# Performance work log

Measured on AMD Instinct MI355X. Metric: run time of the kernel, lower is better.

The kernel has to match this reference:

```python
import jax, jax.numpy as jnp
import numpy as np

B, T = 256, 256
D_TEXT, D_AUDIO, D_VISION = 300, 74, 35
D = D_TEXT + D_AUDIO + D_VISION  # 409
H = 1024
CELL = 512
OUT = 1


def setup_inputs() -> dict:
    key = jax.random.key(0)
    ks = jax.random.split(key, 8)
    s_ih = 1.0 / np.sqrt(H)
    return {
        "x_text": jax.random.normal(ks[0], (B, T, D_TEXT), jnp.float32),
        "x_audio": jax.random.normal(ks[1], (B, T, D_AUDIO), jnp.float32),
        "x_vision": jax.random.normal(ks[2], (B, T, D_VISION), jnp.float32),
        "W_ih": jax.random.normal(ks[3], (4 * H, D), jnp.float32) * s_ih,
        "W_hh": jax.random.normal(ks[4], (4 * H, H), jnp.float32) * s_ih,
        "b_ih": jnp.zeros((4 * H,), jnp.float32),
        "b_hh": jnp.zeros((4 * H,), jnp.float32),
        "W1": jax.random.normal(ks[5], (CELL, H), jnp.float32) / np.sqrt(H),
        "b1": jnp.zeros((CELL,), jnp.float32),
        "W2": jax.random.normal(ks[6], (OUT, CELL), jnp.float32) / np.sqrt(CELL),
        "b2": jnp.zeros((OUT,), jnp.float32),
    }


def _lstm_mlp(x_text, x_audio, x_vision, W_ih, W_hh, b_ih, b_hh, W1, b1, W2, b2):
    # concat modalities along feature dim: [B, T, D]
    x = jnp.concatenate([x_text, x_audio, x_vision], axis=2)
    b = x.shape[0]
    h0 = jnp.zeros((b, H), x.dtype)
    c0 = jnp.zeros((b, H), x.dtype)
    # precompute input-to-gate projection for all timesteps: [T, B, 4H]
    xg = jnp.einsum('btd,gd->tbg', x, W_ih) + (b_ih + b_hh)

    def step(carry, xg_t):
        h, c = carry
        gates = xg_t + h @ W_hh.T  # [B, 4H]
        i, f, g, o = jnp.split(gates, 4, axis=-1)  # PyTorch LSTMCell gate order
        i = jax.nn.sigmoid(i)
        f = jax.nn.sigmoid(f)
        g = jnp.tanh(g)
        o = jax.nn.sigmoid(o)
        c = f * c + i * g
        h = o * jnp.tanh(c)
        return (h, c), None

    (h_last, _), _ = jax.lax.scan(step, (h0, c0), xg)
    # SimpleNet: Linear -> ReLU -> Dropout(eval: identity) -> Linear
    hidden = jax.nn.relu(h_last @ W1.T + b1)
    return hidden @ W2.T + b2  # [B, OUT]


def reference(x_text, x_audio, x_vision, W_ih, W_hh, b_ih, b_hh, W1, b1, W2, b2):
    return _lstm_mlp(x_text, x_audio, x_vision, W_ih, W_hh, b_ih, b_hh, W1, b1, W2, b2)
```

## Files before the change

### kernel.cpp

```cpp
#include <hip/hip_runtime.h>
#include <cstdint>
#include <cstddef>


typedef __attribute__((ext_vector_type(8))) short short8;
typedef __attribute__((ext_vector_type(4))) float f32x4;

#define MFMA_BF16(A,B,C) __builtin_amdgcn_mfma_f32_16x16x32_bf16((A),(B),(C),0,0,0)

#define OFF_FLAGS 0u
#define OFF_HBUF0 4096u
#define ZERO_SPAN 528384u
#define OFF_HBUF1 528384u
#define OFF_HFIN  1052672u
#define OFF_HID   2101248u
#define OFF_BIAS  2625536u
#define OFF_WHH   2641920u
#define OFF_WIH   11030528u
#define OFF_XB    14438400u
#define WS_NEED   68964352ull

static __device__ __forceinline__ uint16_t f2bf(float f) {
  uint32_t u = __builtin_bit_cast(uint32_t, f);
  uint32_t r = u + 0x7FFFu + ((u >> 16) & 1u);
  return (uint16_t)(r >> 16);
}
static __device__ __forceinline__ float sigm(float x) {
  return 1.0f / (1.0f + __expf(-x));
}
static __device__ __forceinline__ float tanh_f(float x) {
  float e = __expf(2.0f * x);
  return 1.0f - 2.0f / (e + 1.0f);
}
static __device__ __forceinline__ void gld_lds16_coh(const void* gsrc, void* ldst) {
  __builtin_amdgcn_global_load_lds(
      (const __attribute__((address_space(1))) uint32_t*)gsrc,
      (__attribute__((address_space(3))) uint32_t*)ldst, 16, 0, 0x11);
}
static __device__ __forceinline__ void gld_lds16(const void* gsrc, void* ldst) {
  __builtin_amdgcn_global_load_lds(
      (const __attribute__((address_space(1))) uint32_t*)gsrc,
      (__attribute__((address_space(3))) uint32_t*)ldst, 16, 0, 0);
}

__global__ __launch_bounds__(256) void pack_xb_kernel(
    const float* __restrict__ xt, const float* __restrict__ xa,
    const float* __restrict__ xv, uint16_t* __restrict__ xb)
{
  int id = blockIdx.x * 256 + threadIdx.x;
  int lane = id & 63;
  int rem  = id >> 6;
  int ks = rem % 13;
  int mt = rem / 13;
  int m = mt * 16 + (lane & 15);
  int t = m >> 8;
  int b = m & 255;
  int k0 = ks * 32 + (lane >> 4) * 8;
  size_t base = (size_t)b * 256 + t;
  uint16_t vals[8];
#pragma unroll
  for (int e = 0; e < 8; ++e) {
    int k = k0 + e;
    float v;
    if (k < 300)      v = xt[base * 300 + k];
    else if (k < 374) v = xa[base * 74  + (k - 300)];
    else if (k < 409) v = xv[base * 35  + (k - 374)];
    else              v = 0.0f;
    vals[e] = f2bf(v);
  }
  uint32_t* d32 = (uint32_t*)(xb + (size_t)id * 8);
#pragma unroll
  for (int i = 0; i < 4; ++i)
    d32[i] = (uint32_t)vals[2*i] | ((uint32_t)vals[2*i+1] << 16);
}

__global__ __launch_bounds__(256) void pack_whh_kernel(
    const float* __restrict__ whh, uint16_t* __restrict__ wp)
{
  int id = blockIdx.x * 256 + threadIdx.x;
  int lane = id & 63;
  int ks = (id >> 6) & 31;
  int q  = (id >> 11) & 3;
  int s  = id >> 13;
  int row = q * 1024 + s * 16 + (lane & 15);
  int k0 = ks * 32 + (lane >> 4) * 8;
  const float* src = whh + (size_t)row * 1024 + k0;
  uint16_t vals[8];
#pragma unroll
  for (int e = 0; e < 8; ++e) vals[e] = f2bf(src[e]);
  uint32_t* d32 = (uint32_t*)(wp + (size_t)id * 8);
#pragma unroll
  for (int i = 0; i < 4; ++i)
    d32[i] = (uint32_t)vals[2*i] | ((uint32_t)vals[2*i+1] << 16);
}

__global__ __launch_bounds__(256) void pack_wih_kernel(
    const float* __restrict__ wih, uint16_t* __restrict__ wp)
{
  int id = blockIdx.x * 256 + threadIdx.x;
  int lane = id & 63;
  int rem = id >> 6;
  int ks = rem % 13;
  int nt = rem / 13;
  int n = nt * 16 + (lane & 15);
  int k0 = ks * 32 + (lane >> 4) * 8;
  uint16_t vals[8];
#pragma unroll
  for (int e = 0; e < 8; ++e) {
    int k = k0 + e;
    vals[e] = (k < 409) ? f2bf(wih[(size_t)n * 409 + k]) : (uint16_t)0;
  }
  uint32_t* d32 = (uint32_t*)(wp + (size_t)id * 8);
#pragma unroll
  for (int i = 0; i < 4; ++i)
    d32[i] = (uint32_t)vals[2*i] | ((uint32_t)vals[2*i+1] << 16);
}

__global__ __launch_bounds__(256) void pack_bias_kernel(
    const float* __restrict__ b_ih, const float* __restrict__ b_hh,
    float* __restrict__ bias)
{
  int id = blockIdx.x * 256 + threadIdx.x;
  bias[id] = b_ih[id] + b_hh[id];
}

__global__ __launch_bounds__(256, 1) void scan_kernel(
    const uint16_t* __restrict__ whh_p, const short8* __restrict__ xb,
    const short8* __restrict__ wih, const float* __restrict__ bias,
    uint16_t* __restrict__ hbuf0, uint16_t* __restrict__ hbuf1,
    float* __restrict__ h_final, uint32_t* flags)
{
  extern __shared__ char smem[];
  float* gl = (float*)(smem + 131072);

  const int tid = threadIdx.x;
  const int bid = blockIdx.x;
  const int g = bid >> 6, s = bid & 63;
  const int lane = tid & 63, w = tid >> 6;

  const short8* wstream = (const short8*)(whh_p + (size_t)s * 65536)
                          + ((size_t)w * 32) * 64 + lane;

  const int row_e = tid >> 2;
  const int j_e = (tid & 3) * 4;
  const int R_e = g * 64 + row_e;
  const int col_e = s * 16 + j_e;
  f32x4 c4 = {0.0f, 0.0f, 0.0f, 0.0f};

  size_t hstore_base;
  {
    int cg0 = col_e;
    int ksh = cg0 >> 5, quad = (cg0 >> 3) & 3, e0 = cg0 & 7;
    int mth = row_e >> 4;
    int laneh = quad * 16 + (row_e & 15);
    hstore_base = (((size_t)(g * 4 + mth) * 32 + ksh) * 64 + laneh) * 8 + e0;
  }

  const short8* Afrag = (const short8*)smem;
  const int myflag = g * 64 + lane;

  const int nt = w * 64 + s;
  short8 Bih[13];
  {
    const short8* bsrc = wih + ((size_t)nt * 13) * 64 + lane;
#pragma unroll
    for (int ks = 0; ks < 13; ++ks) Bih[ks] = bsrc[ks * 64];
  }
  const float bv = bias[nt * 16 + (lane & 15)];

  f32x4 xacc[4];
  {
    const short8* gsrc = xb + (((size_t)0 * 16 + g * 4 + w) * 13) * 64 + lane;
    char* ldst = smem + (size_t)w * 13 * 1024;
#pragma unroll
    for (int p = 0; p < 13; ++p)
      gld_lds16(gsrc + (size_t)p * 64, ldst + p * 1024);
    __syncthreads();
#pragma unroll
    for (int a = 0; a < 4; ++a) { f32x4 v = {bv, bv, bv, bv}; xacc[a] = v; }
#pragma unroll
    for (int kk = 0; kk < 13; ++kk)
#pragma unroll
      for (int a = 0; a < 4; ++a)
        xacc[a] = MFMA_BF16(Afrag[(a * 13 + kk) * 64 + lane], Bih[kk], xacc[a]);
    __syncthreads();
  }

#pragma unroll 1
  for (int ts = 0; ts < 256; ++ts) {
    const uint16_t* hin = (ts & 1) ? hbuf1 : hbuf0;
    uint16_t* hout = (ts & 1) ? hbuf0 : hbuf1;

    {
      const uint16_t* gbase = hin + (size_t)g * 65536
                              + (size_t)(w * 32) * 512 + (size_t)lane * 8;
      char* lbase = smem + (size_t)(w * 32) * 1024;
#pragma unroll
      for (int p = 0; p < 32; ++p)
        gld_lds16_coh(gbase + (size_t)p * 512, lbase + p * 1024);
    }

    f32x4 acc[4];
#pragma unroll
    for (int a = 0; a < 4; ++a) acc[a] = xacc[a];

    __syncthreads();

#pragma unroll
    for (int ks = 0; ks < 32; ++ks) {
      short8 W = wstream[ks * 64];
      short8 A0 = Afrag[(0 * 32 + ks) * 64 + lane];
      short8 A1 = Afrag[(1 * 32 + ks) * 64 + lane];
      short8 A2 = Afrag[(2 * 32 + ks) * 64 + lane];
      short8 A3 = Afrag[(3 * 32 + ks) * 64 + lane];
      acc[0] = MFMA_BF16(A0, W, acc[0]);
      acc[1] = MFMA_BF16(A1, W, acc[1]);
      acc[2] = MFMA_BF16(A2, W, acc[2]);
      acc[3] = MFMA_BF16(A3, W, acc[3]);
    }

    {
      int r0 = (lane >> 4) * 4;
      int cc = lane & 15;
      int colc = w * 16 + cc;
#pragma unroll
      for (int a = 0; a < 4; ++a)
#pragma unroll
        for (int r = 0; r < 4; ++r)
          gl[(a * 16 + r0 + r) * 68 + colc] = acc[a][r];
    }
    __syncthreads();

    if (ts < 255) {
      const short8* gsrc =
          xb + (((size_t)(ts + 1) * 16 + g * 4 + w) * 13) * 64 + lane;
      char* ldst = smem + (size_t)w * 13 * 1024;
#pragma unroll
      for (int p = 0; p < 13; ++p)
        gld_lds16(gsrc + (size_t)p * 64, ldst + p * 1024);
    }

    float hv[4];
#pragma unroll
    for (int u = 0; u < 4; ++u) {
      int cj = j_e + u;
      float xi = gl[row_e * 68 + cj];
      float xf = gl[row_e * 68 + 16 + cj];
      float xg_ = gl[row_e * 68 + 32 + cj];
      float xo = gl[row_e * 68 + 48 + cj];
      float cn = sigm(xf) * c4[u] + sigm(xi) * tanh_f(xg_);
      c4[u] = cn;
      hv[u] = sigm(xo) * tanh_f(cn);
    }
    {
      uint32_t w0 = (uint32_t)f2bf(hv[0]) | ((uint32_t)f2bf(hv[1]) << 16);
      uint32_t w1 = (uint32_t)f2bf(hv[2]) | ((uint32_t)f2bf(hv[3]) << 16);
      unsigned long long v = ((unsigned long long)w1 << 32) | w0;
      __hip_atomic_store((unsigned long long*)(hout + hstore_base), v,
                         __ATOMIC_RELAXED, __HIP_MEMORY_SCOPE_AGENT);
    }
    if (ts == 255) {
      f32x4 hh = {hv[0], hv[1], hv[2], hv[3]};
      *(f32x4*)(h_final + (size_t)R_e * 1024 + col_e) = hh;
    } else {
      __syncthreads();
      if (tid == 0) {
        __hip_atomic_store(&flags[bid], (uint32_t)(ts + 1),
                           __ATOMIC_RELAXED, __HIP_MEMORY_SCOPE_AGENT);
      }
#pragma unroll
      for (int a = 0; a < 4; ++a) { f32x4 v = {bv, bv, bv, bv}; xacc[a] = v; }
#pragma unroll
      for (int kk = 0; kk < 13; ++kk)
#pragma unroll
        for (int a = 0; a < 4; ++a)
          xacc[a] =
              MFMA_BF16(Afrag[(a * 13 + kk) * 64 + lane], Bih[kk], xacc[a]);
      __syncthreads();
      while (__hip_atomic_load(&flags[myflag], __ATOMIC_RELAXED,
                               __HIP_MEMORY_SCOPE_AGENT) < (uint32_t)(ts + 1)) {
        __builtin_amdgcn_s_sleep(1);
      }
    }
  }
}

__global__ __launch_bounds__(256) void mlp1_kernel(
    const float* __restrict__ h_final, const float* __restrict__ W1,
    const float* __restrict__ b1, float* __restrict__ hidden)
{
  __shared__ float hl[8 * 1024];
  __shared__ float part[4 * 64 * 8];
  int tid = threadIdx.x;
  int rb = blockIdx.x;
  int cb = blockIdx.y;
  const f32x4* hsrc = (const f32x4*)(h_final + (size_t)rb * 8 * 1024);
  for (int i = tid; i < 2048; i += 256) ((f32x4*)hl)[i] = hsrc[i];
  __syncthreads();
  int cell_l = tid & 63;
  int kq = tid >> 6;
  int cell = cb * 64 + cell_l;
  float accv[8] = {0,0,0,0,0,0,0,0};
  const f32x4* wrow = (const f32x4*)(W1 + (size_t)cell * 1024) + kq * 64;
  const f32x4* hl4 = (const f32x4*)hl;
  for (int k4 = 0; k4 < 64; ++k4) {
    f32x4 wv = wrow[k4];
    int kidx = kq * 64 + k4;
#pragma unroll
    for (int r = 0; r < 8; ++r) {
      f32x4 hv = hl4[r * 256 + kidx];
      accv[r] += wv[0] * hv[0] + wv[1] * hv[1] + wv[2] * hv[2] + wv[3] * hv[3];
    }
  }
#pragma unroll
  for (int r = 0; r < 8; ++r) part[(kq * 64 + cell_l) * 8 + r] = accv[r];
  __syncthreads();
#pragma unroll
  for (int rr = 0; rr < 2; ++rr) {
    int r = kq * 2 + rr;
    float sum = b1[cell];
    for (int q = 0; q < 4; ++q) sum += part[(q * 64 + cell_l) * 8 + r];
    hidden[(size_t)(rb * 8 + r) * 512 + cell] = fmaxf(sum, 0.0f);
  }
}

__global__ __launch_bounds__(256) void mlp2_kernel(
    const float* __restrict__ hidden, const float* __restrict__ W2,
    const float* __restrict__ b2, float* __restrict__ out)
{
  __shared__ float w2l[512];
  int tid = threadIdx.x;
  for (int i = tid; i < 512; i += 256) w2l[i] = W2[i];
  __syncthreads();
  const f32x4* hrow = (const f32x4*)(hidden + (size_t)tid * 512);
  const f32x4* w4 = (const f32x4*)w2l;
  float acc = b2[0];
  for (int k = 0; k < 128; ++k) {
    f32x4 a = hrow[k], b = w4[k];
    acc += a[0] * b[0] + a[1] * b[1] + a[2] * b[2] + a[3] * b[3];
  }
  out[tid] = acc;
}

extern "C" void kernel_launch(void* const* d_in, const int* in_sizes, int n_in,
                              void* d_out, int out_size, void* d_ws, size_t ws_size,
                              hipStream_t stream)
{
  (void)in_sizes; (void)n_in; (void)out_size;
  if (ws_size < WS_NEED) return;

  const float* xt   = (const float*)d_in[0];
  const float* xa   = (const float*)d_in[1];
  const float* xv   = (const float*)d_in[2];
  const float* W_ih = (const float*)d_in[3];
  const float* W_hh = (const float*)d_in[4];
  const float* b_ih = (const float*)d_in[5];
  const float* b_hh = (const float*)d_in[6];
  const float* W1   = (const float*)d_in[7];
  const float* b1   = (const float*)d_in[8];
  const float* W2   = (const float*)d_in[9];
  const float* b2   = (const float*)d_in[10];
  float* out = (float*)d_out;
  char* ws = (char*)d_ws;

  uint32_t* flags   = (uint32_t*)(ws + OFF_FLAGS);
  uint16_t* hb0     = (uint16_t*)(ws + OFF_HBUF0);
  uint16_t* hb1     = (uint16_t*)(ws + OFF_HBUF1);
  float*    h_final = (float*)(ws + OFF_HFIN);
  float*    hidden  = (float*)(ws + OFF_HID);
  float*    bias    = (float*)(ws + OFF_BIAS);
  uint16_t* whh_p   = (uint16_t*)(ws + OFF_WHH);
  uint16_t* wih_p   = (uint16_t*)(ws + OFF_WIH);
  uint16_t* xb      = (uint16_t*)(ws + OFF_XB);

  hipFuncSetAttribute((const void*)scan_kernel,
                      hipFuncAttributeMaxDynamicSharedMemorySize, 148480);

  hipMemsetAsync(ws, 0, ZERO_SPAN, stream);

  pack_xb_kernel  <<<13312, 256, 0, stream>>>(xt, xa, xv, xb);
  pack_whh_kernel <<<2048,  256, 0, stream>>>(W_hh, whh_p);
  pack_wih_kernel <<<832,   256, 0, stream>>>(W_ih, wih_p);
  pack_bias_kernel<<<16,    256, 0, stream>>>(b_ih, b_hh, bias);

  scan_kernel<<<256, 256, 148480, stream>>>(
      whh_p, (const short8*)xb, (const short8*)wih_p, bias,
      hb0, hb1, h_final, flags);

  mlp1_kernel<<<dim3(32, 8), 256, 0, stream>>>(h_final, W1, b1, hidden);
  mlp2_kernel<<<1, 256, 0, stream>>>(hidden, W2, b2, out);
}
```

Before: 1.910 ms.

## Retile LSTM scan blocks to 32 rows by 2 column tiles

Changes the persistent scan kernel's block decomposition from 4 batch-row groups by 64 column slices to 8 batch-row groups by 32 slices. Each block now handles 32 batch rows and 32 hidden columns, so the h tile it loads into LDS each step and its shared memory footprint are halved. Each W_hh stream element now feeds two MFMAs instead of four, so W_hh is streamed 8 times per step instead of 4. The flag wait now depends on 32 producer blocks rather than 64, and the per-warp 2x2 MFMA tiles may improve register reuse.

After: 1.851 ms. -3.1%, faster.

```diff
diff --git a/kernel.cpp b/kernel.cpp
--- a/kernel.cpp
+++ b/kernel.cpp
@@ -131,20 +131,22 @@
     float* __restrict__ h_final, uint32_t* flags)
 {
   extern __shared__ char smem[];
-  float* gl = (float*)(smem + 131072);
+  float* gl = (float*)(smem + 65536);
 
   const int tid = threadIdx.x;
   const int bid = blockIdx.x;
-  const int g = bid >> 6, s = bid & 63;
-  const int lane = tid & 63, w = tid >> 6;
-
-  const short8* wstream = (const short8*)(whh_p + (size_t)s * 65536)
-                          + ((size_t)w * 32) * 64 + lane;
-
-  const int row_e = tid >> 2;
-  const int j_e = (tid & 3) * 4;
-  const int R_e = g * 64 + row_e;
-  const int col_e = s * 16 + j_e;
+  const int g = bid >> 5, s2 = bid & 31;
+  const int lane = tid & 63, q = tid >> 6;
+
+  const short8* ws0 = (const short8*)whh_p
+                      + (size_t)(s2 * 2 + 0) * 8192 + (size_t)q * 2048 + lane;
+  const short8* ws1 = (const short8*)whh_p
+                      + (size_t)(s2 * 2 + 1) * 8192 + (size_t)q * 2048 + lane;
+
+  const int row_e = tid >> 3;
+  const int j_e = (tid & 7) * 4;
+  const int R_e = g * 32 + row_e;
+  const int col_e = s2 * 32 + j_e;
   f32x4 c4 = {0.0f, 0.0f, 0.0f, 0.0f};
 
   size_t hstore_base;
@@ -153,36 +155,43 @@
     int ksh = cg0 >> 5, quad = (cg0 >> 3) & 3, e0 = cg0 & 7;
     int mth = row_e >> 4;
     int laneh = quad * 16 + (row_e & 15);
-    hstore_base = (((size_t)(g * 4 + mth) * 32 + ksh) * 64 + laneh) * 8 + e0;
+    hstore_base = (((size_t)(g * 2 + mth) * 32 + ksh) * 64 + laneh) * 8 + e0;
   }
 
   const short8* Afrag = (const short8*)smem;
-  const int myflag = g * 64 + lane;
-
-  const int nt = w * 64 + s;
-  short8 Bih[13];
+  const int myflag = g * 32 + (lane & 31);
+
+  short8 Bih0[13], Bih1[13];
   {
-    const short8* bsrc = wih + ((size_t)nt * 13) * 64 + lane;
-#pragma unroll
-    for (int ks = 0; ks < 13; ++ks) Bih[ks] = bsrc[ks * 64];
-  }
-  const float bv = bias[nt * 16 + (lane & 15)];
-
-  f32x4 xacc[4];
+    const short8* b0 = wih + ((size_t)(q * 64 + s2 * 2 + 0) * 13) * 64 + lane;
+    const short8* b1 = wih + ((size_t)(q * 64 + s2 * 2 + 1) * 13) * 64 + lane;
+#pragma unroll
+    for (int ks = 0; ks < 13; ++ks) { Bih0[ks] = b0[ks * 64]; Bih1[ks] = b1[ks * 64]; }
+  }
+  const float bv0 = bias[q * 1024 + (s2 * 2 + 0) * 16 + (lane & 15)];
+  const float bv1 = bias[q * 1024 + (s2 * 2 + 1) * 16 + (lane & 15)];
+
+  f32x4 xacc00, xacc01, xacc10, xacc11;
   {
-    const short8* gsrc = xb + (((size_t)0 * 16 + g * 4 + w) * 13) * 64 + lane;
-    char* ldst = smem + (size_t)w * 13 * 1024;
-#pragma unroll
-    for (int p = 0; p < 13; ++p)
-      gld_lds16(gsrc + (size_t)p * 64, ldst + p * 1024);
+    if (q < 2) {
+      const short8* gsrc = xb + ((size_t)(g * 2 + q)) * 832 + lane;
+      char* ldst = smem + (size_t)q * 13312;
+#pragma unroll
+      for (int p = 0; p < 13; ++p)
+        gld_lds16(gsrc + (size_t)p * 64, ldst + p * 1024);
+    }
     __syncthreads();
-#pragma unroll
-    for (int a = 0; a < 4; ++a) { f32x4 v = {bv, bv, bv, bv}; xacc[a] = v; }
-#pragma unroll
-    for (int kk = 0; kk < 13; ++kk)
-#pragma unroll
-      for (int a = 0; a < 4; ++a)
-        xacc[a] = MFMA_BF16(Afrag[(a * 13 + kk) * 64 + lane], Bih[kk], xacc[a]);
+    f32x4 v0 = {bv0, bv0, bv0, bv0}, v1 = {bv1, bv1, bv1, bv1};
+    xacc00 = v0; xacc01 = v1; xacc10 = v0; xacc11 = v1;
+#pragma unroll
+    for (int kk = 0; kk < 13; ++kk) {
+      short8 A0 = Afrag[kk * 64 + lane];
+      short8 A1 = Afrag[832 + kk * 64 + lane];
+      xacc00 = MFMA_BF16(A0, Bih0[kk], xacc00);
+      xacc01 = MFMA_BF16(A0, Bih1[kk], xacc01);
+      xacc10 = MFMA_BF16(A1, Bih0[kk], xacc10);
+      xacc11 = MFMA_BF16(A1, Bih1[kk], xacc11);
+    }
     __syncthreads();
   }
 
@@ -192,49 +201,47 @@
     uint16_t* hout = (ts & 1) ? hbuf0 : hbuf1;
 
     {
-      const uint16_t* gbase = hin + (size_t)g * 65536
-                              + (size_t)(w * 32) * 512 + (size_t)lane * 8;
-      char* lbase = smem + (size_t)(w * 32) * 1024;
-#pragma unroll
-      for (int p = 0; p < 32; ++p)
+      const uint16_t* gbase = hin + (size_t)g * 32768
+                              + (size_t)q * 8192 + (size_t)lane * 8;
+      char* lbase = smem + (size_t)q * 16384;
+#pragma unroll
+      for (int p = 0; p < 16; ++p)
         gld_lds16_coh(gbase + (size_t)p * 512, lbase + p * 1024);
     }
 
-    f32x4 acc[4];
-#pragma unroll
-    for (int a = 0; a < 4; ++a) acc[a] = xacc[a];
+    f32x4 acc00 = xacc00, acc01 = xacc01, acc10 = xacc10, acc11 = xacc11;
 
     __syncthreads();
 
 #pragma unroll
     for (int ks = 0; ks < 32; ++ks) {
-      short8 W = wstream[ks * 64];
+      short8 W0 = ws0[ks * 64];
+      short8 W1 = ws1[ks * 64];
       short8 A0 = Afrag[(0 * 32 + ks) * 64 + lane];
       short8 A1 = Afrag[(1 * 32 + ks) * 64 + lane];
-      short8 A2 = Afrag[(2 * 32 + ks) * 64 + lane];
-      short8 A3 = Afrag[(3 * 32 + ks) * 64 + lane];
-      acc[0] = MFMA_BF16(A0, W, acc[0]);
-      acc[1] = MFMA_BF16(A1, W, acc[1]);
-      acc[2] = MFMA_BF16(A2, W, acc[2]);
-      acc[3] = MFMA_BF16(A3, W, acc[3]);
+      acc00 = MFMA_BF16(A0, W0, acc00);
+      acc01 = MFMA_BF16(A0, W1, acc01);
+      acc10 = MFMA_BF16(A1, W0, acc10);
+      acc11 = MFMA_BF16(A1, W1, acc11);
     }
 
     {
       int r0 = (lane >> 4) * 4;
       int cc = lane & 15;
-      int colc = w * 16 + cc;
-#pragma unroll
-      for (int a = 0; a < 4; ++a)
-#pragma unroll
-        for (int r = 0; r < 4; ++r)
-          gl[(a * 16 + r0 + r) * 68 + colc] = acc[a][r];
+#pragma unroll
+      for (int r = 0; r < 4; ++r) {
+        gl[(0 * 16 + r0 + r) * 132 + q * 32 +  0 + cc] = acc00[r];
+        gl[(0 * 16 + r0 + r) * 132 + q * 32 + 16 + cc] = acc01[r];
+        gl[(1 * 16 + r0 + r) * 132 + q * 32 +  0 + cc] = acc10[r];
+        gl[(1 * 16 + r0 + r) * 132 + q * 32 + 16 + cc] = acc11[r];
+      }
     }
     __syncthreads();
 
-    if (ts < 255) {
+    if (ts < 255 && q < 2) {
       const short8* gsrc =
-          xb + (((size_t)(ts + 1) * 16 + g * 4 + w) * 13) * 64 + lane;
-      char* ldst = smem + (size_t)w * 13 * 1024;
+          xb + ((size_t)(ts + 1) * 16 + g * 2 + q) * 832 + lane;
+      char* ldst = smem + (size_t)q * 13312;
 #pragma unroll
       for (int p = 0; p < 13; ++p)
         gld_lds16(gsrc + (size_t)p * 64, ldst + p * 1024);
@@ -243,11 +250,11 @@
     float hv[4];
 #pragma unroll
     for (int u = 0; u < 4; ++u) {
-      int cj = j_e + u;
-      float xi = gl[row_e * 68 + cj];
-      float xf = gl[row_e * 68 + 16 + cj];
-      float xg_ = gl[row_e * 68 + 32 + cj];
-      float xo = gl[row_e * 68 + 48 + cj];
+      int c = j_e + u;
+      float xi  = gl[row_e * 132 +  0 + c];
+      float xf  = gl[row_e * 132 + 32 + c];
+      float xg_ = gl[row_e * 132 + 64 + c];
+      float xo  = gl[row_e * 132 + 96 + c];
       float cn = sigm(xf) * c4[u] + sigm(xi) * tanh_f(xg_);
       c4[u] = cn;
       hv[u] = sigm(xo) * tanh_f(cn);
@@ -268,14 +275,19 @@
         __hip_atomic_store(&flags[bid], (uint32_t)(ts + 1),
                            __ATOMIC_RELAXED, __HIP_MEMORY_SCOPE_AGENT);
       }
-#pragma unroll
-      for (int a = 0; a < 4; ++a) { f32x4 v = {bv, bv, bv, bv}; xacc[a] = v; }
-#pragma unroll
-      for (int kk = 0; kk < 13; ++kk)
-#pragma unroll
-        for (int a = 0; a < 4; ++a)
-          xacc[a] =
-              MFMA_BF16(Afrag[(a * 13 + kk) * 64 + lane], Bih[kk], xacc[a]);
+      {
+        f32x4 v0 = {bv0, bv0, bv0, bv0}, v1 = {bv1, bv1, bv1, bv1};
+        xacc00 = v0; xacc01 = v1; xacc10 = v0; xacc11 = v1;
+#pragma unroll
+        for (int kk = 0; kk < 13; ++kk) {
+          short8 A0 = Afrag[kk * 64 + lane];
+          short8 A1 = Afrag[832 + kk * 64 + lane];
+          xacc00 = MFMA_BF16(A0, Bih0[kk], xacc00);
+          xacc01 = MFMA_BF16(A0, Bih1[kk], xacc01);
+          xacc10 = MFMA_BF16(A1, Bih0[kk], xacc10);
+          xacc11 = MFMA_BF16(A1, Bih1[kk], xacc11);
+        }
+      }
       __syncthreads();
       while (__hip_atomic_load(&flags[myflag], __ATOMIC_RELAXED,
                                __HIP_MEMORY_SCOPE_AGENT) < (uint32_t)(ts + 1)) {
@@ -374,7 +386,7 @@
   uint16_t* xb      = (uint16_t*)(ws + OFF_XB);
 
   hipFuncSetAttribute((const void*)scan_kernel,
-                      hipFuncAttributeMaxDynamicSharedMemorySize, 148480);
+                      hipFuncAttributeMaxDynamicSharedMemorySize, 82432);
 
   hipMemsetAsync(ws, 0, ZERO_SPAN, stream);
 
@@ -383,7 +395,7 @@
   pack_wih_kernel <<<832,   256, 0, stream>>>(W_ih, wih_p);
   pack_bias_kernel<<<16,    256, 0, stream>>>(b_ih, b_hh, bias);
 
-  scan_kernel<<<256, 256, 148480, stream>>>(
+  scan_kernel<<<256, 256, 82432, stream>>>(
       whh_p, (const short8*)xb, (const short8*)wih_p, bias,
       hb0, hb1, h_final, flags);
 
```
